# Kernel tuning notes

Measured on AMD Instinct MI355X. Metric: run time of the kernel, lower is better.

Reference implementation:

```python
import jax, jax.numpy as jnp
import numpy as np

STRIDE = 15           # cfg.shm.dilation_kernel
PAD = STRIDE // 2
P = 1048576           # cfg.shm.max_n_pixel (static sparse-pixel budget)


def dilate(alpha):
    # mask = (0.01 < alpha < 0.99); then 15x15 max-pool, stride 1, pad 7 (same size)
    m = jnp.logical_and(alpha > 0.01, alpha < 0.99).astype(alpha.dtype)
    return jax.lax.reduce_window(
        m, -jnp.inf, jax.lax.max,
        (1, 1, STRIDE, STRIDE), (1, 1, 1, 1),
        [(0, 0), (0, 0), (PAD, PAD), (PAD, PAD)])


def setup_inputs() -> dict:
    key = jax.random.key(0)
    ks = jax.random.split(key, 8)
    d = 128
    return {
        'image': jax.random.normal(ks[0], (8, 3, 512, 512), jnp.float32),
        'lr_pred': jax.random.uniform(ks[1], (8, 1, 512, 512), jnp.float32),
        'W1': jax.random.normal(ks[2], (4, d), jnp.float32) * 0.5,
        'b1': jnp.zeros((d,), jnp.float32),
        'W2': jax.random.normal(ks[3], (d, d), jnp.float32) * (1.0 / np.sqrt(d)),
        'b2': jnp.zeros((d,), jnp.float32),
        'W3': jax.random.normal(ks[4], (d, 1), jnp.float32) * (1.0 / np.sqrt(d)),
        'b3': jnp.zeros((1,), jnp.float32),
    }


def reference(image, lr_pred, W1, b1, W2, b2, W3, b3):
    B, C, H, W = image.shape
    mask = dilate(lr_pred)                       # [B,1,H,W] dilated uncertainty mask

    # generate_sparse_inputs: cat(img, (lr_pred-0.5)/0.5) channels-last, gather where mask>0
    feat = jnp.concatenate([image, (lr_pred - 0.5) / 0.5], axis=1)  # [B,4,H,W]
    feat = feat.transpose(0, 2, 3, 1).reshape(-1, C + 1)            # [B*H*W, 4]
    mflat = mask.reshape(-1)                                        # [B*H*W]

    (idx,) = jnp.nonzero(mflat > 0, size=P, fill_value=0)           # static-size gather
    count = jnp.sum(mflat > 0)
    valid = (jnp.arange(P) < count).astype(feat.dtype)              # [P]

    # torch's generate_sparse_inputs runs under no_grad -> stop_gradient on gather
    x = jax.lax.stop_gradient(feat[idx])                            # [P,4]

    # stand-in sparse head (shm): per-pixel MLP with sigmoid alpha output
    h = jax.nn.relu(x @ W1 + b1)
    h = jax.nn.relu(h @ W2 + b2)
    pred = jax.nn.sigmoid(h @ W3 + b3)[:, 0]                        # [P]

    # scatter predictions back to dense grid; ungathered masked pixels keep lr_pred
    scattered = jnp.zeros_like(mflat).at[idx].add(pred * valid)
    covered = jnp.zeros_like(mflat).at[idx].add(valid)
    lrf = lr_pred.reshape(-1)
    dense = scattered + (1.0 - covered) * lrf

    # final blend: pred*mask + lr_pred*(1-mask)
    final = dense * mflat + lrf * (1.0 - mflat)
    return final.reshape(B, 1, H, W)
```

## Files before the change

kernel.cpp:

```cpp
#include <hip/hip_runtime.h>
#include <hip/hip_bf16.h>
#include <math.h>

#define BB 8
#define HH 512
#define WW 512
#define NPIX (BB * HH * WW)
#define HWPIX (HH * WW)
#define PBUD 1048576
#define RAD 7
#define NB (NPIX / 256)
#define NMLP (NPIX / 128)

#define XOFF  32768
#define ZROW  (XOFF + 2048)
#define FLAGS (XOFF + 2064)

typedef __attribute__((ext_vector_type(4))) float f32x4;
typedef __attribute__((ext_vector_type(8))) short short8;
typedef __attribute__((ext_vector_type(2))) unsigned int u32x2;
typedef __attribute__((ext_vector_type(4))) unsigned int u32x4;

__device__ __forceinline__ unsigned short f2bf(float f) {
    unsigned int u = __float_as_uint(f);
    unsigned int r = (u + 0x7fffu + ((u >> 16) & 1u)) >> 16;
    return (unsigned short)r;
}

__device__ __forceinline__ unsigned int pkbf(float a, float b) {
    __hip_bfloat162 h = __float22bfloat162_rn(make_float2(a, b));
    return *(unsigned int*)&h;
}

__global__ void k_prep(const float* __restrict__ w2, const float* __restrict__ w1,
                       const float* __restrict__ b1,
                       unsigned short* __restrict__ w2f, unsigned short* __restrict__ w1f) {
    int i = blockIdx.x * 256 + threadIdx.x;
    if (i < 16384) {
        int e  = i & 7;
        int l  = (i >> 3) & 63;
        int ks = (i >> 9) & 3;
        int jc = i >> 11;
        int j = jc * 16 + (l & 15);
        int k = ks * 32 + ((l >> 4) & 3) * 8 + e;
        w2f[i] = f2bf(w2[k * 128 + j]);
    } else {
        int i2 = i - 16384;
        int e  = i2 & 7;
        int l  = (i2 >> 3) & 63;
        int fi = i2 >> 9;
        int j = fi * 16 + (l & 15);
        int k = ((l >> 4) & 3) * 8 + e;
        float v = (k < 4) ? w1[k * 128 + j] : ((k == 4) ? b1[j] : 0.0f);
        w1f[i2] = f2bf(v);
    }
}

__global__ void k_rowdil(const float* __restrict__ lr, unsigned char* __restrict__ rowdil) {
    int p = blockIdx.x * 256 + threadIdx.x;
    int w = p & (WW - 1);
    int row0 = p - w;
    int lo = w - RAD; if (lo < 0) lo = 0;
    int hi = w + RAD; if (hi > WW - 1) hi = WW - 1;
    unsigned char any = 0;
    for (int x = lo; x <= hi; ++x) {
        float v = lr[row0 + x];
        any |= (unsigned char)(v > 0.01f && v < 0.99f);
    }
    rowdil[p] = any;
}

__global__ void k_coldil(const unsigned char* __restrict__ rowdil,
                         unsigned char* __restrict__ dm,
                         unsigned char* __restrict__ rankb,
                         int* __restrict__ gsum) {
    int p = blockIdx.x * 256 + threadIdx.x;
    int h = (p >> 9) & (HH - 1);
    int lo = h - RAD; if (lo < 0) lo = 0;
    int hi = h + RAD; if (hi > HH - 1) hi = HH - 1;
    lo -= h; hi -= h;
    unsigned char any = 0;
    for (int d = lo; d <= hi; ++d) any |= rowdil[p + d * WW];
    dm[p] = any;

    unsigned long long bal = __ballot(any != 0);
    __shared__ int wsum[4];
    int lane = threadIdx.x & 63;
    int wid  = threadIdx.x >> 6;
    if (lane == 0) wsum[wid] = __popcll(bal);
    __syncthreads();
    int pre = __popcll(bal & ((1ull << lane) - 1ull));
    int woff = 0;
    for (int i = 0; i < wid; ++i) woff += wsum[i];
    rankb[p] = (unsigned char)(woff + pre);
    if (threadIdx.x == 0) gsum[blockIdx.x] = wsum[0] + wsum[1] + wsum[2] + wsum[3];
}

__global__ void k_scan(const int* __restrict__ gsum, int* __restrict__ goff) {
    __shared__ int tsum[1024];
    int t = threadIdx.x;
    int base = t * 8;
    int v[8];
    int s = 0;
#pragma unroll
    for (int i = 0; i < 8; ++i) { v[i] = gsum[base + i]; s += v[i]; }
    tsum[t] = s;
    __syncthreads();
    for (int off = 1; off < 1024; off <<= 1) {
        int x = tsum[t];
        int y = (t >= off) ? tsum[t - off] : 0;
        __syncthreads();
        tsum[t] = x + y;
        __syncthreads();
    }
    int run = (t == 0) ? 0 : tsum[t - 1];
#pragma unroll
    for (int i = 0; i < 8; ++i) { goff[base + i] = run; run += v[i]; }
}

__global__ __launch_bounds__(256, 4)
void k_mlp(const float* __restrict__ image, const float* __restrict__ lr,
           const unsigned short* __restrict__ w1f, const unsigned short* __restrict__ w2f,
           const float* __restrict__ b2, const float* __restrict__ w3,
           const float* __restrict__ b3,
           const unsigned char* __restrict__ dm, const unsigned char* __restrict__ rankb,
           const int* __restrict__ goff, float* __restrict__ out) {
    __shared__ __align__(16) char lds[34944];
    int p0 = blockIdx.x * 128;
    int t  = threadIdx.x;
    int w    = t >> 6;
    int l    = t & 63;
    int lr16 = l & 15;
    int lh   = l >> 4;

    const short8* wf1 = (const short8*)w1f;
    short8 a1[8];
#pragma unroll
    for (int jt = 0; jt < 8; ++jt) a1[jt] = wf1[jt * 64 + l];

    bool  sel = false;
    float lrv = 0.f;
    if (t < 128) {
        int p = p0 + t;
        lrv = lr[p];
        sel = dm[p] && (goff[p >> 8] + (int)rankb[p] < PBUD);
        size_t bimg = (size_t)(p >> 18) * 3 * HWPIX + (p & (HWPIX - 1));
        float x0 = image[bimg];
        float x1 = image[bimg + HWPIX];
        float x2 = image[bimg + 2 * HWPIX];
        float x3 = 2.0f * lrv - 1.0f;
        u32x4 d0 = { pkbf(x0, x1), pkbf(x2, x3), pkbf(1.0f, 0.0f), 0u };
        *(u32x4*)(lds + XOFF + t * 16) = d0;
        unsigned long long bal = __ballot(sel);
        if (l == 0) *(int*)(lds + FLAGS + w * 4) = (bal != 0ull) ? 1 : 0;
    }
    if (t == 128) *(u32x4*)(lds + ZROW) = (u32x4){0u, 0u, 0u, 0u};
    __syncthreads();
    int any = *(const int*)(lds + FLAGS) | *(const int*)(lds + FLAGS + 4);
    if (!any) {
        if (t < 128) out[p0 + t] = lrv;
        return;
    }

    int pxb = w * 32;
#pragma unroll
    for (int pxt = 0; pxt < 2; ++pxt) {
        int px = pxb + pxt * 16 + lr16;
        const char* xaddr = (lh == 0) ? (lds + XOFF + px * 16) : (lds + ZROW);
        short8 xb = *(const short8*)xaddr;
#pragma unroll
        for (int jt = 0; jt < 8; ++jt) {
            f32x4 c = {0.f, 0.f, 0.f, 0.f};
            c = __builtin_amdgcn_mfma_f32_16x16x32_bf16(a1[jt], xb, c, 0, 0, 0);
            int j0 = jt * 16 + lh * 4;
            u32x2 u = { pkbf(fmaxf(c[0], 0.f), fmaxf(c[1], 0.f)),
                        pkbf(fmaxf(c[2], 0.f), fmaxf(c[3], 0.f)) };
            *(u32x2*)(lds + (((px << 8) | (j0 << 1)) ^ ((px & 15) << 4))) = u;
        }
    }

    int rowbase = pxb;
    short8 af[2][4];
#pragma unroll
    for (int ks = 0; ks < 4; ++ks) {
#pragma unroll
        for (int mt = 0; mt < 2; ++mt) {
            int row = rowbase + mt * 16 + lr16;
            int a = (((row << 8) | (ks << 6) | (lh << 4))) ^ ((row & 15) << 4);
            af[mt][ks] = *(const short8*)(lds + a);
        }
    }

    float b2v[8], w3v[8];
#pragma unroll
    for (int jc = 0; jc < 8; ++jc) {
        int col = jc * 16 + lr16;
        b2v[jc] = b2[col];
        w3v[jc] = w3[col];
    }
    float b3v = b3[0];

    f32x4 acc[2][8];
#pragma unroll
    for (int mt = 0; mt < 2; ++mt)
#pragma unroll
        for (int jc = 0; jc < 8; ++jc)
            acc[mt][jc] = (f32x4){b2v[jc], b2v[jc], b2v[jc], b2v[jc]};

    const short8* wf = (const short8*)w2f;
#pragma unroll
    for (int jc = 0; jc < 8; ++jc) {
        short8 bf[4];
#pragma unroll
        for (int ks = 0; ks < 4; ++ks) bf[ks] = wf[(jc * 4 + ks) * 64 + l];
#pragma unroll
        for (int ks = 0; ks < 4; ++ks) {
            acc[0][jc] = __builtin_amdgcn_mfma_f32_16x16x32_bf16(af[0][ks], bf[ks], acc[0][jc], 0, 0, 0);
            acc[1][jc] = __builtin_amdgcn_mfma_f32_16x16x32_bf16(af[1][ks], bf[ks], acc[1][jc], 0, 0, 0);
        }
    }

#pragma unroll
    for (int mt = 0; mt < 2; ++mt) {
#pragma unroll
        for (int r = 0; r < 4; ++r) {
            int row = rowbase + mt * 16 + lh * 4 + r;
            float part = 0.f;
#pragma unroll
            for (int jc = 0; jc < 8; ++jc)
                part += fmaxf(acc[mt][jc][r], 0.f) * w3v[jc];
            part += __shfl_xor(part, 1);
            part += __shfl_xor(part, 2);
            part += __shfl_xor(part, 4);
            part += __shfl_xor(part, 8);
            if (lr16 == 0) {
                int p = p0 + row;
                float lrvp = lr[p];
                bool s = dm[p] && (goff[p >> 8] + (int)rankb[p] < PBUD);
                float logit = b3v + part;
                out[p] = s ? (1.0f / (1.0f + __expf(-logit))) : lrvp;
            }
        }
    }
}

extern "C" void kernel_launch(void* const* d_in, const int* in_sizes, int n_in,
                              void* d_out, int out_size, void* d_ws, size_t ws_size,
                              hipStream_t stream) {
    const float* image = (const float*)d_in[0];
    const float* lr    = (const float*)d_in[1];
    const float* w1    = (const float*)d_in[2];
    const float* b1    = (const float*)d_in[3];
    const float* w2    = (const float*)d_in[4];
    const float* b2    = (const float*)d_in[5];
    const float* w3    = (const float*)d_in[6];
    const float* b3    = (const float*)d_in[7];
    float* out = (float*)d_out;

    char* ws = (char*)d_ws;
    unsigned char* rowdil = (unsigned char*)ws;
    unsigned char* dm     = (unsigned char*)(ws + (size_t)NPIX);
    unsigned char* rankb  = (unsigned char*)(ws + 2 * (size_t)NPIX);
    int* gsum             = (int*)(ws + 3 * (size_t)NPIX);
    int* goff             = (int*)(ws + 3 * (size_t)NPIX + NB * 4);
    unsigned short* w2f   = (unsigned short*)(ws + 3 * (size_t)NPIX + 2 * NB * 4);
    unsigned short* w1f   = w2f + 16384;

    k_prep  <<<80, 256, 0, stream>>>(w2, w1, b1, w2f, w1f);
    k_rowdil<<<NPIX / 256, 256, 0, stream>>>(lr, rowdil);
    k_coldil<<<NB, 256, 0, stream>>>(rowdil, dm, rankb, gsum);
    k_scan  <<<1, 1024, 0, stream>>>(gsum, goff);
    k_mlp   <<<NMLP, 256, 0, stream>>>(image, lr, w1f, w2f, b2, w3, b3,
                                       dm, rankb, goff, out);
}
```

Baseline: 140.2 us.

## Compact active pixel blocks in scan and launch MLP only over them

The scan kernel now also builds a compacted list of 256-pixel blocks that contain selected pixels within budget. A separate vectorized copy kernel writes lr_pred to the output, and the MLP kernel indexes blocks through the active list, exiting early for surplus blocks and writing only selected pixels. Input features are packed directly into registers instead of staged through LDS. This aims to cut wasted work on inactive blocks, at the cost of an extra full-size copy pass, a second scan in the single-block scan kernel, and a full grid launch that mostly exits immediately.

```diff
diff --git a/kernel.cpp b/kernel.cpp
--- a/kernel.cpp
+++ b/kernel.cpp
@@ -12,14 +12,10 @@
 #define NB (NPIX / 256)
 #define NMLP (NPIX / 128)
 
-#define XOFF  32768
-#define ZROW  (XOFF + 2048)
-#define FLAGS (XOFF + 2064)
-
 typedef __attribute__((ext_vector_type(4))) float f32x4;
+typedef __attribute__((ext_vector_type(4))) float float4v;
 typedef __attribute__((ext_vector_type(8))) short short8;
 typedef __attribute__((ext_vector_type(2))) unsigned int u32x2;
-typedef __attribute__((ext_vector_type(4))) unsigned int u32x4;
 
 __device__ __forceinline__ unsigned short f2bf(float f) {
     unsigned int u = __float_as_uint(f);
@@ -96,7 +92,8 @@
     if (threadIdx.x == 0) gsum[blockIdx.x] = wsum[0] + wsum[1] + wsum[2] + wsum[3];
 }
 
-__global__ void k_scan(const int* __restrict__ gsum, int* __restrict__ goff) {
+__global__ void k_scan(const int* __restrict__ gsum, int* __restrict__ goff,
+                       int* __restrict__ act, int* __restrict__ act_n) {
     __shared__ int tsum[1024];
     int t = threadIdx.x;
     int base = t * 8;
@@ -114,72 +111,104 @@
         __syncthreads();
     }
     int run = (t == 0) ? 0 : tsum[t - 1];
-#pragma unroll
-    for (int i = 0; i < 8; ++i) { goff[base + i] = run; run += v[i]; }
+    int aflag[8];
+    int acnt = 0;
+#pragma unroll
+    for (int i = 0; i < 8; ++i) {
+        goff[base + i] = run;
+        aflag[i] = (v[i] > 0 && run < PBUD) ? 1 : 0;
+        acnt += aflag[i];
+        run += v[i];
+    }
+    __syncthreads();
+    tsum[t] = acnt;
+    __syncthreads();
+    for (int off = 1; off < 1024; off <<= 1) {
+        int x = tsum[t];
+        int y = (t >= off) ? tsum[t - off] : 0;
+        __syncthreads();
+        tsum[t] = x + y;
+        __syncthreads();
+    }
+    int aoff = tsum[t] - acnt;
+    if (t == 1023) act_n[0] = tsum[1023];
+#pragma unroll
+    for (int i = 0; i < 8; ++i)
+        if (aflag[i]) act[aoff++] = base + i;
+}
+
+__global__ void k_copy(const float* __restrict__ lr, float* __restrict__ out) {
+    int i = (blockIdx.x * 256 + threadIdx.x) * 4;
+    *(float4v*)(out + i) = *(const float4v*)(lr + i);
 }
 
 __global__ __launch_bounds__(256, 4)
-void k_mlp(const float* __restrict__ image, const float* __restrict__ lr,
-           const unsigned short* __restrict__ w1f, const unsigned short* __restrict__ w2f,
-           const float* __restrict__ b2, const float* __restrict__ w3,
-           const float* __restrict__ b3,
-           const unsigned char* __restrict__ dm, const unsigned char* __restrict__ rankb,
-           const int* __restrict__ goff, float* __restrict__ out) {
-    __shared__ __align__(16) char lds[34944];
-    int p0 = blockIdx.x * 128;
-    int t  = threadIdx.x;
+void k_mlpw(const float* __restrict__ image, const float* __restrict__ lr,
+            const unsigned short* __restrict__ w1f, const unsigned short* __restrict__ w2f,
+            const float* __restrict__ b2, const float* __restrict__ w3,
+            const float* __restrict__ b3,
+            const unsigned char* __restrict__ dm, const unsigned char* __restrict__ rankb,
+            const int* __restrict__ goff, const int* __restrict__ act,
+            const int* __restrict__ act_n, float* __restrict__ out) {
+    int ab   = blockIdx.x >> 1;
+    if (ab >= act_n[0]) return;
+    int half = blockIdx.x & 1;
+    int p0   = act[ab] * 256 + half * 128;
+
+    __shared__ __align__(16) char lds[32768];
+    int t    = threadIdx.x;
     int w    = t >> 6;
     int l    = t & 63;
     int lr16 = l & 15;
     int lh   = l >> 4;
+    int p0w  = p0 + w * 32;
 
     const short8* wf1 = (const short8*)w1f;
     short8 a1[8];
 #pragma unroll
     for (int jt = 0; jt < 8; ++jt) a1[jt] = wf1[jt * 64 + l];
 
-    bool  sel = false;
-    float lrv = 0.f;
-    if (t < 128) {
-        int p = p0 + t;
-        lrv = lr[p];
-        sel = dm[p] && (goff[p >> 8] + (int)rankb[p] < PBUD);
-        size_t bimg = (size_t)(p >> 18) * 3 * HWPIX + (p & (HWPIX - 1));
-        float x0 = image[bimg];
-        float x1 = image[bimg + HWPIX];
-        float x2 = image[bimg + 2 * HWPIX];
-        float x3 = 2.0f * lrv - 1.0f;
-        u32x4 d0 = { pkbf(x0, x1), pkbf(x2, x3), pkbf(1.0f, 0.0f), 0u };
-        *(u32x4*)(lds + XOFF + t * 16) = d0;
-        unsigned long long bal = __ballot(sel);
-        if (l == 0) *(int*)(lds + FLAGS + w * 4) = (bal != 0ull) ? 1 : 0;
-    }
-    if (t == 128) *(u32x4*)(lds + ZROW) = (u32x4){0u, 0u, 0u, 0u};
-    __syncthreads();
-    int any = *(const int*)(lds + FLAGS) | *(const int*)(lds + FLAGS + 4);
-    if (!any) {
-        if (t < 128) out[p0 + t] = lrv;
-        return;
-    }
-
-    int pxb = w * 32;
+    short8 xb[2];
 #pragma unroll
     for (int pxt = 0; pxt < 2; ++pxt) {
-        int px = pxb + pxt * 16 + lr16;
-        const char* xaddr = (lh == 0) ? (lds + XOFF + px * 16) : (lds + ZROW);
-        short8 xb = *(const short8*)xaddr;
-#pragma unroll
-        for (int jt = 0; jt < 8; ++jt) {
-            f32x4 c = {0.f, 0.f, 0.f, 0.f};
-            c = __builtin_amdgcn_mfma_f32_16x16x32_bf16(a1[jt], xb, c, 0, 0, 0);
-            int j0 = jt * 16 + lh * 4;
-            u32x2 u = { pkbf(fmaxf(c[0], 0.f), fmaxf(c[1], 0.f)),
-                        pkbf(fmaxf(c[2], 0.f), fmaxf(c[3], 0.f)) };
-            *(u32x2*)(lds + (((px << 8) | (j0 << 1)) ^ ((px & 15) << 4))) = u;
-        }
-    }
-
-    int rowbase = pxb;
+        unsigned int uu[4] = {0u, 0u, 0u, 0u};
+        if (l < 16) {
+            int pp = p0w + pxt * 16 + l;
+            float lrv = lr[pp];
+            size_t bimg = (size_t)(pp >> 18) * 3 * HWPIX + (pp & (HWPIX - 1));
+            float x0 = image[bimg];
+            float x1 = image[bimg + HWPIX];
+            float x2 = image[bimg + 2 * HWPIX];
+            float x3 = 2.0f * lrv - 1.0f;
+            uu[0] = pkbf(x0, x1);
+            uu[1] = pkbf(x2, x3);
+            uu[2] = pkbf(1.0f, 0.0f);
+        }
+        xb[pxt] = *(short8*)uu;
+    }
+
+#pragma unroll
+    for (int jt = 0; jt < 8; ++jt) {
+        f32x4 c0 = {0.f, 0.f, 0.f, 0.f};
+        f32x4 c1 = {0.f, 0.f, 0.f, 0.f};
+        c0 = __builtin_amdgcn_mfma_f32_16x16x32_bf16(a1[jt], xb[0], c0, 0, 0, 0);
+        c1 = __builtin_amdgcn_mfma_f32_16x16x32_bf16(a1[jt], xb[1], c1, 0, 0, 0);
+        int j0 = jt * 16 + lh * 4;
+        {
+            int pxb = w * 32 + lr16;
+            u32x2 u = { pkbf(fmaxf(c0[0], 0.f), fmaxf(c0[1], 0.f)),
+                        pkbf(fmaxf(c0[2], 0.f), fmaxf(c0[3], 0.f)) };
+            *(u32x2*)(lds + (((pxb << 8) | (j0 << 1)) ^ ((pxb & 15) << 4))) = u;
+        }
+        {
+            int pxb = w * 32 + 16 + lr16;
+            u32x2 u = { pkbf(fmaxf(c1[0], 0.f), fmaxf(c1[1], 0.f)),
+                        pkbf(fmaxf(c1[2], 0.f), fmaxf(c1[3], 0.f)) };
+            *(u32x2*)(lds + (((pxb << 8) | (j0 << 1)) ^ ((pxb & 15) << 4))) = u;
+        }
+    }
+
+    int rowbase = w * 32;
     short8 af[2][4];
 #pragma unroll
     for (int ks = 0; ks < 4; ++ks) {
@@ -234,11 +263,12 @@
             part += __shfl_xor(part, 4);
             part += __shfl_xor(part, 8);
             if (lr16 == 0) {
-                int p = p0 + row;
-                float lrvp = lr[p];
-                bool s = dm[p] && (goff[p >> 8] + (int)rankb[p] < PBUD);
-                float logit = b3v + part;
-                out[p] = s ? (1.0f / (1.0f + __expf(-logit))) : lrvp;
+                int pp = p0 + row;
+                bool ss = dm[pp] && (goff[pp >> 8] + (int)rankb[pp] < PBUD);
+                if (ss) {
+                    float logit = b3v + part;
+                    out[pp] = 1.0f / (1.0f + __expf(-logit));
+                }
             }
         }
     }
@@ -263,13 +293,16 @@
     unsigned char* rankb  = (unsigned char*)(ws + 2 * (size_t)NPIX);
     int* gsum             = (int*)(ws + 3 * (size_t)NPIX);
     int* goff             = (int*)(ws + 3 * (size_t)NPIX + NB * 4);
-    unsigned short* w2f   = (unsigned short*)(ws + 3 * (size_t)NPIX + 2 * NB * 4);
+    int* act              = (int*)(ws + 3 * (size_t)NPIX + 2 * NB * 4);
+    int* act_n            = (int*)(ws + 3 * (size_t)NPIX + 3 * NB * 4);
+    unsigned short* w2f   = (unsigned short*)(ws + 3 * (size_t)NPIX + 3 * NB * 4 + 16);
     unsigned short* w1f   = w2f + 16384;
 
     k_prep  <<<80, 256, 0, stream>>>(w2, w1, b1, w2f, w1f);
     k_rowdil<<<NPIX / 256, 256, 0, stream>>>(lr, rowdil);
     k_coldil<<<NB, 256, 0, stream>>>(rowdil, dm, rankb, gsum);
-    k_scan  <<<1, 1024, 0, stream>>>(gsum, goff);
-    k_mlp   <<<NMLP, 256, 0, stream>>>(image, lr, w1f, w2f, b2, w3, b3,
-                                       dm, rankb, goff, out);
-}
+    k_scan  <<<1, 1024, 0, stream>>>(gsum, goff, act, act_n);
+    k_copy  <<<NPIX / 1024, 256, 0, stream>>>(lr, out);
+    k_mlpw  <<<NMLP, 256, 0, stream>>>(image, lr, w1f, w2f, b2, w3, b3,
+                                       dm, rankb, goff, act, act_n, out);
+}
```

Result: slower. 149.3 us (+6.5%).
